# Optimization experiments

Hardware: AMD Instinct MI355X
Metric: run time of the kernel (lower is better)

## Reference

```python
import jax, jax.numpy as jnp
import numpy as np

B, S, D_MODEL = 2, 2048, 2048
HQ, HKV = 16, 8
HEAD_DIM = D_MODEL // HQ  # 128
ROPE_THETA = 10000.0


def setup_inputs() -> dict:
    key = jax.random.key(0)
    ks = jax.random.split(key, 5)
    scale = 1.0 / np.sqrt(D_MODEL)
    x = jax.random.normal(ks[0], (B, S, D_MODEL), dtype=jnp.float32)
    # torch nn.Linear weights: [out_features, in_features], no bias
    wq = jax.random.normal(ks[1], (HQ * HEAD_DIM, D_MODEL), dtype=jnp.float32) * scale
    wk = jax.random.normal(ks[2], (HKV * HEAD_DIM, D_MODEL), dtype=jnp.float32) * scale
    wv = jax.random.normal(ks[3], (HKV * HEAD_DIM, D_MODEL), dtype=jnp.float32) * scale
    wo = jax.random.normal(ks[4], (D_MODEL, HQ * HEAD_DIM), dtype=jnp.float32) * scale
    return {"x": x, "wq": wq, "wk": wk, "wv": wv, "wo": wo}


def _rope_tables(seq_len, head_dim, theta, dtype):
    # freqs = 1/theta^(2i/d); polar table equivalent to view_as_complex rotation
    inv = 1.0 / (theta ** (jnp.arange(0, head_dim, 2, dtype=jnp.float32) / head_dim))
    t = jnp.arange(seq_len, dtype=jnp.float32)
    ang = jnp.outer(t, inv)  # [S, head_dim//2]
    return jnp.cos(ang).astype(dtype), jnp.sin(ang).astype(dtype)


def _apply_rope(x, cos, sin):
    # x: [B, S, H, D]; complex pairs are interleaved (even=real, odd=imag)
    xr, xi = x[..., 0::2], x[..., 1::2]
    c = cos[None, :, None, :]
    s = sin[None, :, None, :]
    out_r = xr * c - xi * s
    out_i = xr * s + xi * c
    return jnp.stack([out_r, out_i], axis=-1).reshape(x.shape)


def reference(x, wq, wk, wv, wo):
    b, s, _ = x.shape
    q = (x @ wq.T).reshape(b, s, HQ, HEAD_DIM)
    k = (x @ wk.T).reshape(b, s, HKV, HEAD_DIM)
    v = (x @ wv.T).reshape(b, s, HKV, HEAD_DIM)

    cos, sin = _rope_tables(s, HEAD_DIM, ROPE_THETA, x.dtype)
    q = _apply_rope(q, cos, sin)
    k = _apply_rope(k, cos, sin)

    # [B, H, S, D]
    q = q.transpose(0, 2, 1, 3)
    k = k.transpose(0, 2, 1, 3)
    v = v.transpose(0, 2, 1, 3)
    # GQA: repeat kv heads to match query heads
    g = HQ // HKV
    k = jnp.repeat(k, g, axis=1)
    v = jnp.repeat(v, g, axis=1)

    scale = 1.0 / jnp.sqrt(jnp.asarray(HEAD_DIM, dtype=x.dtype))
    scores = jnp.einsum("bhqd,bhkd->bhqk", q, k) * scale
    causal = jnp.tril(jnp.ones((s, s), dtype=bool))
    scores = jnp.where(causal[None, None], scores, jnp.asarray(-jnp.inf, scores.dtype))
    attn = jax.nn.softmax(scores, axis=-1)
    out = jnp.einsum("bhqk,bhkd->bhqd", attn, v)  # [B, H, S, D]
    out = out.transpose(0, 2, 1, 3).reshape(b, s, HQ * HEAD_DIM)
    return out @ wo.T
```

## Files before the change

### kernel.cpp

```cpp
#include <hip/hip_runtime.h>

#define S_LEN 2048
#define DM    2048
#define HQ_N  16
#define HKV_N 8
#define HD    128

typedef unsigned short u16;
typedef unsigned int   u32;
typedef short bf16x8 __attribute__((ext_vector_type(8)));
typedef float f32x4  __attribute__((ext_vector_type(4)));
typedef u16   u16x8  __attribute__((ext_vector_type(8)));

__device__ __forceinline__ float b2f(u16 u) {
  u32 x = ((u32)u) << 16;
  return __builtin_bit_cast(float, x);
}
__device__ __forceinline__ u16 f2b(float f) {
  u32 u = __builtin_bit_cast(u32, f);
  u32 r = u + 0x7fffu + ((u >> 16) & 1u);
  return (u16)(r >> 16);
}

#define GLOAD_LDS16(g, l)                                                     \
  __builtin_amdgcn_global_load_lds(                                           \
      (const __attribute__((address_space(1))) void*)(g),                     \
      (__attribute__((address_space(3))) void*)(l), 16, 0, 0)

__global__ void cvt_bf16(const float* __restrict__ src, u16* __restrict__ dst) {
  int id = blockIdx.x * blockDim.x + threadIdx.x;
  float4 a = ((const float4*)src)[id * 2];
  float4 b = ((const float4*)src)[id * 2 + 1];
  u16x8 o;
  o[0] = f2b(a.x); o[1] = f2b(a.y); o[2] = f2b(a.z); o[3] = f2b(a.w);
  o[4] = f2b(b.x); o[5] = f2b(b.y); o[6] = f2b(b.z); o[7] = f2b(b.w);
  ((u16x8*)dst)[id] = o;
}

__global__ void rope_tables(float* __restrict__ cosT, float* __restrict__ sinT) {
  int id = blockIdx.x * blockDim.x + threadIdx.x;
  int t = id >> 6, i = id & 63;
  float inv = (float)pow(10000.0, -(double)(2 * i) / 128.0);
  float ang = (float)t * inv;
  cosT[id] = cosf(ang);
  sinT[id] = sinf(ang);
}

template <int EPI, int HH>
__global__ __launch_bounds__(256) void gemm_bt(const u16* __restrict__ A,
                                               const u16* __restrict__ W,
                                               void* __restrict__ Cv,
                                               int M, int N, int K) {
  __shared__ alignas(16) u16 As[128 * 32];
  __shared__ alignas(16) u16 Bs[128 * 32];
  const int tid  = threadIdx.x;
  const int lane = tid & 63;
  const int wave = tid >> 6;
  const int wr = (wave >> 1) * 64;
  const int wc = (wave & 1) * 64;
  const int bm = blockIdx.y * 128;
  const int bn = blockIdx.x * 128;
  const int r0 = tid >> 2;
  const int c0 = (tid & 3) * 8;
  u16* AsD = &As[tid * 8];
  u16* BsD = &Bs[tid * 8];
  const u16* Ap = A + (size_t)(bm + r0) * K + c0;
  const u16* Wp = W + (size_t)(bn + r0) * K + c0;
  const int cl = lane & 15;
  const int g8 = (lane >> 4) * 8;
  f32x4 acc[4][4] = {};
  for (int k0 = 0; k0 < K; k0 += 32) {
    __syncthreads();
    GLOAD_LDS16(Ap + k0, AsD);
    GLOAD_LDS16(Ap + (size_t)64 * K + k0, AsD + 2048);
    GLOAD_LDS16(Wp + k0, BsD);
    GLOAD_LDS16(Wp + (size_t)64 * K + k0, BsD + 2048);
    __syncthreads();
    bf16x8 af[4], bfr[4];
#pragma unroll
    for (int m = 0; m < 4; ++m)
      af[m] = *(const bf16x8*)&As[(wr + m * 16 + cl) * 32 + g8];
#pragma unroll
    for (int n = 0; n < 4; ++n)
      bfr[n] = *(const bf16x8*)&Bs[(wc + n * 16 + cl) * 32 + g8];
#pragma unroll
    for (int m = 0; m < 4; ++m)
#pragma unroll
      for (int n = 0; n < 4; ++n)
        acc[m][n] = __builtin_amdgcn_mfma_f32_16x16x32_bf16(af[m], bfr[n], acc[m][n], 0, 0, 0);
  }
  const int g4 = (lane >> 4) * 4;
#pragma unroll
  for (int m = 0; m < 4; ++m)
#pragma unroll
    for (int n = 0; n < 4; ++n)
#pragma unroll
      for (int r = 0; r < 4; ++r) {
        int row = bm + wr + m * 16 + g4 + r;
        int col = bn + wc + n * 16 + cl;
        float fv = acc[m][n][r];
        if (EPI == 3) {
          ((float*)Cv)[(size_t)row * N + col] = fv;
        } else if (EPI == 1) {
          int bb = row >> 11, s = row & (S_LEN - 1);
          int hk = col >> 7, d = col & (HD - 1);
          ((u16*)Cv)[((size_t)((bb * HKV_N + hk) * HD + d)) * S_LEN + s] = f2b(fv);
        } else {
          int bb = row >> 11, s = row & (S_LEN - 1);
          int h = col >> 7, d = col & (HD - 1);
          ((u16*)Cv)[((size_t)((bb * HH + h) * S_LEN + s)) * HD + d] = f2b(fv);
        }
      }
}

__global__ void rope_inplace(u16* __restrict__ buf,
                             const float* __restrict__ cosT,
                             const float* __restrict__ sinT, float scale) {
  int id = blockIdx.x * blockDim.x + threadIdx.x;
  int d0 = (id & 15) * 8;
  int rs = id >> 4;
  int s = rs & (S_LEN - 1);
  u16* p = buf + (size_t)rs * HD + d0;
  u16x8 v = *(const u16x8*)p;
  int p0 = d0 >> 1;
  float4 c  = *(const float4*)(cosT + s * 64 + p0);
  float4 sn = *(const float4*)(sinT + s * 64 + p0);
  float cc[4] = {c.x, c.y, c.z, c.w};
  float ss[4] = {sn.x, sn.y, sn.z, sn.w};
  u16x8 o;
#pragma unroll
  for (int j = 0; j < 4; ++j) {
    float x0 = b2f(v[2 * j]), x1 = b2f(v[2 * j + 1]);
    o[2 * j]     = f2b((x0 * cc[j] - x1 * ss[j]) * scale);
    o[2 * j + 1] = f2b((x0 * ss[j] + x1 * cc[j]) * scale);
  }
  *(u16x8*)p = o;
}

__global__ __launch_bounds__(256, 4) void attn_fwd(const u16* __restrict__ Q,
                                                   const u16* __restrict__ Kh,
                                                   const u16* __restrict__ Vt,
                                                   u16* __restrict__ O) {
  __shared__ alignas(16) u16 Ks[64 * 128];
  __shared__ alignas(16) u16 Vs[128 * 64];
  __shared__ alignas(16) u16 Plds[4][2][16 * 32];
  const int tid  = threadIdx.x;
  const int wave = tid >> 6;
  const int lane = tid & 63;
  const int orig = (blockIdx.x & 7) * 128 + (blockIdx.x >> 3);
  const int bh = orig >> 5;
  const int j = orig & 31;
  const int qblk = (j & 1) ? ((j - 1) >> 1) : (31 - (j >> 1));
  const int bb = bh >> 4, h = bh & 15;
  const int bkv = bb * HKV_N + (h >> 1);
  const u16* Kp = Kh + (size_t)bkv * S_LEN * HD;
  const u16* Vp = Vt + (size_t)bkv * HD * S_LEN;
  const int cl = lane & 15;
  const int gr = lane >> 4;
  const int g8 = gr * 8;
  const int sw8 = (cl & 7) << 3;
  const int q0w = qblk * 64 + wave * 16;
  const u16* Qp = Q + ((size_t)bh * S_LEN + q0w) * HD;
  bf16x8 qf[4];
#pragma unroll
  for (int c = 0; c < 4; ++c)
    qf[c] = *(const bf16x8*)&Qp[cl * HD + c * 32 + g8];
  const int krow_w = wave * 4 + gr;
  const int kcol = (cl * 8) ^ ((krow_w & 7) << 3);
  const u16* kSrc = Kp + (size_t)krow_w * HD + kcol;
  const int vrow_w = wave * 8 + (lane >> 3);
  const int vcol = ((lane & 7) * 8) ^ (((lane >> 3) & 7) << 3);
  const u16* vSrc = Vp + (size_t)vrow_w * S_LEN + vcol;
  float m[4]    = {-1e30f, -1e30f, -1e30f, -1e30f};
  float lsum[4] = {0.f, 0.f, 0.f, 0.f};
  f32x4 oacc[8] = {};
  u16* Pw0 = &Plds[wave][0][0];
  u16* Pw1 = &Plds[wave][1][0];
  for (int t = 0; t <= qblk; ++t) {
    const int k0 = t * 64;
    __syncthreads();
#pragma unroll
    for (int j2 = 0; j2 < 4; ++j2)
      GLOAD_LDS16(kSrc + (size_t)(k0 + j2 * 16) * HD, &Ks[(j2 * 4 + wave) * 512]);
#pragma unroll
    for (int j2 = 0; j2 < 4; ++j2)
      GLOAD_LDS16(vSrc + (size_t)j2 * 32 * S_LEN + k0, &Vs[(j2 * 4 + wave) * 512]);
    __syncthreads();
    f32x4 sc[4] = {{0.f, 0.f, 0.f, 0.f}, {0.f, 0.f, 0.f, 0.f},
                   {0.f, 0.f, 0.f, 0.f}, {0.f, 0.f, 0.f, 0.f}};
#pragma unroll
    for (int c = 0; c < 4; ++c) {
      const int kq = (c * 32 + g8) ^ sw8;
#pragma unroll
      for (int ks = 0; ks < 4; ++ks) {
        bf16x8 kf = *(const bf16x8*)&Ks[(ks * 16 + cl) * 128 + kq];
        sc[ks] = __builtin_amdgcn_mfma_f32_16x16x32_bf16(qf[c], kf, sc[ks], 0, 0, 0);
      }
    }
    float corr[4];
    if (t == qblk) {
#pragma unroll
      for (int r = 0; r < 4; ++r) {
        const int qrel = wave * 16 + gr * 4 + r;
#pragma unroll
        for (int ks = 0; ks < 4; ++ks)
          if (ks * 16 + cl > qrel) sc[ks][r] = -1e30f;
      }
    }
#pragma unroll
    for (int r = 0; r < 4; ++r) {
      float mx = fmaxf(fmaxf(sc[0][r], sc[1][r]), fmaxf(sc[2][r], sc[3][r]));
#pragma unroll
      for (int off = 1; off < 16; off <<= 1)
        mx = fmaxf(mx, __shfl_xor(mx, off));
      const float mn = fmaxf(m[r], mx);
      corr[r] = __expf(m[r] - mn);
      float p0 = __expf(sc[0][r] - mn);
      float p1 = __expf(sc[1][r] - mn);
      float p2 = __expf(sc[2][r] - mn);
      float p3 = __expf(sc[3][r] - mn);
      float rs = (p0 + p1) + (p2 + p3);
#pragma unroll
      for (int off = 1; off < 16; off <<= 1)
        rs += __shfl_xor(rs, off);
      lsum[r] = lsum[r] * corr[r] + rs;
      m[r] = mn;
      const int row = gr * 4 + r;
      Pw0[row * 32 + cl]      = f2b(p0);
      Pw0[row * 32 + 16 + cl] = f2b(p1);
      Pw1[row * 32 + cl]      = f2b(p2);
      Pw1[row * 32 + 16 + cl] = f2b(p3);
    }
#pragma unroll
    for (int nd = 0; nd < 8; ++nd)
#pragma unroll
      for (int r = 0; r < 4; ++r) oacc[nd][r] *= corr[r];
    __builtin_amdgcn_sched_barrier(0);
    asm volatile("s_waitcnt lgkmcnt(0)" ::: "memory");
    __builtin_amdgcn_sched_barrier(0);
    bf16x8 pa0 = *(const bf16x8*)&Pw0[cl * 32 + g8];
    bf16x8 pa1 = *(const bf16x8*)&Pw1[cl * 32 + g8];
    const int vq0 = g8 ^ sw8;
    const int vq1 = (32 + g8) ^ sw8;
#pragma unroll
    for (int nd = 0; nd < 8; ++nd) {
      bf16x8 vf0 = *(const bf16x8*)&Vs[(nd * 16 + cl) * 64 + vq0];
      bf16x8 vf1 = *(const bf16x8*)&Vs[(nd * 16 + cl) * 64 + vq1];
      oacc[nd] = __builtin_amdgcn_mfma_f32_16x16x32_bf16(pa0, vf0, oacc[nd], 0, 0, 0);
      oacc[nd] = __builtin_amdgcn_mfma_f32_16x16x32_bf16(pa1, vf1, oacc[nd], 0, 0, 0);
    }
  }
#pragma unroll
  for (int r = 0; r < 4; ++r) {
    const int q = q0w + gr * 4 + r;
    const float inv = 1.0f / lsum[r];
#pragma unroll
    for (int nd = 0; nd < 8; ++nd)
      O[(((size_t)bb * S_LEN + q) * HQ_N + h) * HD + nd * 16 + cl] =
          f2b(oacc[nd][r] * inv);
  }
}

extern "C" void kernel_launch(void* const* d_in, const int* in_sizes, int n_in,
                              void* d_out, int out_size, void* d_ws, size_t ws_size,
                              hipStream_t stream) {
  (void)in_sizes; (void)n_in; (void)out_size; (void)ws_size;
  const float* x  = (const float*)d_in[0];
  const float* wq = (const float*)d_in[1];
  const float* wk = (const float*)d_in[2];
  const float* wv = (const float*)d_in[3];
  const float* wo = (const float*)d_in[4];
  float* out = (float*)d_out;
  char* w = (char*)d_ws;
  u16*  Qh   = (u16*)(w + 0);
  u16*  Kh   = (u16*)(w + 16777216);
  u16*  Vt   = (u16*)(w + 25165824);
  u16*  x16  = (u16*)(w + 33554432);
  u16*  wq16 = (u16*)(w + 50331648);
  u16*  wk16 = (u16*)(w + 58720256);
  u16*  wv16 = (u16*)(w + 62914560);
  float* cosT = (float*)(w + 67108864);
  float* sinT = (float*)(w + 67633152);
  u16* wo16 = wq16;
  u16* attnout = x16;

  rope_tables<<<512, 256, 0, stream>>>(cosT, sinT);
  cvt_bf16<<<4096, 256, 0, stream>>>(x,  x16);
  cvt_bf16<<<2048, 256, 0, stream>>>(wq, wq16);
  cvt_bf16<<<1024, 256, 0, stream>>>(wk, wk16);
  cvt_bf16<<<1024, 256, 0, stream>>>(wv, wv16);
  gemm_bt<2, 16><<<dim3(16, 32), 256, 0, stream>>>(x16, wq16, Qh, 4096, 2048, 2048);
  gemm_bt<2, 8> <<<dim3(8, 32),  256, 0, stream>>>(x16, wk16, Kh, 4096, 1024, 2048);
  gemm_bt<1, 8> <<<dim3(8, 32),  256, 0, stream>>>(x16, wv16, Vt, 4096, 1024, 2048);
  cvt_bf16<<<2048, 256, 0, stream>>>(wo, wo16);
  rope_inplace<<<4096, 256, 0, stream>>>(Qh, cosT, sinT, 0.08838834764831845f);
  rope_inplace<<<2048, 256, 0, stream>>>(Kh, cosT, sinT, 1.0f);
  attn_fwd<<<1024, 256, 0, stream>>>(Qh, Kh, Vt, attnout);
  gemm_bt<3, 16><<<dim3(16, 32), 256, 0, stream>>>(attnout, wo16, out, 4096, 2048, 2048);
}
```

Baseline: 486.0 us.

## Fuse Q, K, V projections into one GEMM with XCD-aware block remap

Merges the three separate QKV projection GEMMs into a single launch over a concatenated bf16 weight buffer, with the epilogue routing each column block to the Q, K or V layout. Block indices are remapped so consecutive blocks spread across the 8 XCDs, which aims to improve L2 reuse of the shared A and W tiles. This removes two kernel launches and the tail effects of the smaller K/V grids. It adds branching in the epilogue and relies on the weights being contiguous in the workspace.

New measurement: 455.3 us. 6.3% less time.

```diff
diff --git a/kernel.cpp b/kernel.cpp
--- a/kernel.cpp
+++ b/kernel.cpp
@@ -46,11 +46,79 @@
   sinT[id] = sinf(ang);
 }
 
-template <int EPI, int HH>
-__global__ __launch_bounds__(256) void gemm_bt(const u16* __restrict__ A,
-                                               const u16* __restrict__ W,
-                                               void* __restrict__ Cv,
-                                               int M, int N, int K) {
+__global__ __launch_bounds__(256) void gemm_qkv(const u16* __restrict__ A,
+                                                const u16* __restrict__ W,
+                                                u16* __restrict__ Qh,
+                                                u16* __restrict__ Kh,
+                                                u16* __restrict__ Vt) {
+  __shared__ alignas(16) u16 As[128 * 32];
+  __shared__ alignas(16) u16 Bs[128 * 32];
+  const int K = DM;
+  const int tid  = threadIdx.x;
+  const int lane = tid & 63;
+  const int wave = tid >> 6;
+  const int wr = (wave >> 1) * 64;
+  const int wc = (wave & 1) * 64;
+  const int orig = (blockIdx.x & 7) * 128 + (blockIdx.x >> 3);
+  const int bn = (orig >> 5) * 128;
+  const int bm = (orig & 31) * 128;
+  const int r0 = tid >> 2;
+  const int c0 = (tid & 3) * 8;
+  u16* AsD = &As[tid * 8];
+  u16* BsD = &Bs[tid * 8];
+  const u16* Ap = A + (size_t)(bm + r0) * K + c0;
+  const u16* Wp = W + (size_t)(bn + r0) * K + c0;
+  const int cl = lane & 15;
+  const int g8 = (lane >> 4) * 8;
+  f32x4 acc[4][4] = {};
+  for (int k0 = 0; k0 < K; k0 += 32) {
+    __syncthreads();
+    GLOAD_LDS16(Ap + k0, AsD);
+    GLOAD_LDS16(Ap + (size_t)64 * K + k0, AsD + 2048);
+    GLOAD_LDS16(Wp + k0, BsD);
+    GLOAD_LDS16(Wp + (size_t)64 * K + k0, BsD + 2048);
+    __syncthreads();
+    bf16x8 af[4], bfr[4];
+#pragma unroll
+    for (int m = 0; m < 4; ++m)
+      af[m] = *(const bf16x8*)&As[(wr + m * 16 + cl) * 32 + g8];
+#pragma unroll
+    for (int n = 0; n < 4; ++n)
+      bfr[n] = *(const bf16x8*)&Bs[(wc + n * 16 + cl) * 32 + g8];
+#pragma unroll
+    for (int m = 0; m < 4; ++m)
+#pragma unroll
+      for (int n = 0; n < 4; ++n)
+        acc[m][n] = __builtin_amdgcn_mfma_f32_16x16x32_bf16(af[m], bfr[n], acc[m][n], 0, 0, 0);
+  }
+  const int g4 = (lane >> 4) * 4;
+#pragma unroll
+  for (int m = 0; m < 4; ++m)
+#pragma unroll
+    for (int n = 0; n < 4; ++n)
+#pragma unroll
+      for (int r = 0; r < 4; ++r) {
+        int row = bm + wr + m * 16 + g4 + r;
+        int col = bn + wc + n * 16 + cl;
+        int bb = row >> 11, s = row & (S_LEN - 1);
+        u16 v = f2b(acc[m][n][r]);
+        if (bn < 2048) {
+          int h = col >> 7, d = col & (HD - 1);
+          Qh[((size_t)((bb * HQ_N + h) * S_LEN + s)) * HD + d] = v;
+        } else if (bn < 3072) {
+          int hk = (col >> 7) - 16, d = col & (HD - 1);
+          Kh[((size_t)((bb * HKV_N + hk) * S_LEN + s)) * HD + d] = v;
+        } else {
+          int hk = (col >> 7) - 24, d = col & (HD - 1);
+          Vt[((size_t)((bb * HKV_N + hk) * HD + d)) * S_LEN + s] = v;
+        }
+      }
+}
+
+__global__ __launch_bounds__(256) void gemm_out(const u16* __restrict__ A,
+                                                const u16* __restrict__ W,
+                                                float* __restrict__ C,
+                                                int M, int N, int K) {
   __shared__ alignas(16) u16 As[128 * 32];
   __shared__ alignas(16) u16 Bs[128 * 32];
   const int tid  = threadIdx.x;
@@ -98,18 +166,7 @@
       for (int r = 0; r < 4; ++r) {
         int row = bm + wr + m * 16 + g4 + r;
         int col = bn + wc + n * 16 + cl;
-        float fv = acc[m][n][r];
-        if (EPI == 3) {
-          ((float*)Cv)[(size_t)row * N + col] = fv;
-        } else if (EPI == 1) {
-          int bb = row >> 11, s = row & (S_LEN - 1);
-          int hk = col >> 7, d = col & (HD - 1);
-          ((u16*)Cv)[((size_t)((bb * HKV_N + hk) * HD + d)) * S_LEN + s] = f2b(fv);
-        } else {
-          int bb = row >> 11, s = row & (S_LEN - 1);
-          int h = col >> 7, d = col & (HD - 1);
-          ((u16*)Cv)[((size_t)((bb * HH + h) * S_LEN + s)) * HD + d] = f2b(fv);
-        }
+        C[(size_t)row * N + col] = acc[m][n][r];
       }
 }
 
@@ -272,29 +329,25 @@
   const float* wo = (const float*)d_in[4];
   float* out = (float*)d_out;
   char* w = (char*)d_ws;
-  u16*  Qh   = (u16*)(w + 0);
-  u16*  Kh   = (u16*)(w + 16777216);
-  u16*  Vt   = (u16*)(w + 25165824);
-  u16*  x16  = (u16*)(w + 33554432);
-  u16*  wq16 = (u16*)(w + 50331648);
-  u16*  wk16 = (u16*)(w + 58720256);
-  u16*  wv16 = (u16*)(w + 62914560);
-  float* cosT = (float*)(w + 67108864);
-  float* sinT = (float*)(w + 67633152);
-  u16* wo16 = wq16;
+  u16*  Qh     = (u16*)(w + 0);
+  u16*  Kh     = (u16*)(w + 16777216);
+  u16*  Vt     = (u16*)(w + 25165824);
+  u16*  x16    = (u16*)(w + 33554432);
+  u16*  wqkv16 = (u16*)(w + 50331648);
+  float* cosT  = (float*)(w + 67108864);
+  float* sinT  = (float*)(w + 67633152);
+  u16* wo16 = wqkv16;
   u16* attnout = x16;
 
   rope_tables<<<512, 256, 0, stream>>>(cosT, sinT);
   cvt_bf16<<<4096, 256, 0, stream>>>(x,  x16);
-  cvt_bf16<<<2048, 256, 0, stream>>>(wq, wq16);
-  cvt_bf16<<<1024, 256, 0, stream>>>(wk, wk16);
-  cvt_bf16<<<1024, 256, 0, stream>>>(wv, wv16);
-  gemm_bt<2, 16><<<dim3(16, 32), 256, 0, stream>>>(x16, wq16, Qh, 4096, 2048, 2048);
-  gemm_bt<2, 8> <<<dim3(8, 32),  256, 0, stream>>>(x16, wk16, Kh, 4096, 1024, 2048);
-  gemm_bt<1, 8> <<<dim3(8, 32),  256, 0, stream>>>(x16, wv16, Vt, 4096, 1024, 2048);
+  cvt_bf16<<<2048, 256, 0, stream>>>(wq, wqkv16);
+  cvt_bf16<<<1024, 256, 0, stream>>>(wk, wqkv16 + 2048 * 2048);
+  cvt_bf16<<<1024, 256, 0, stream>>>(wv, wqkv16 + 3072 * 2048);
+  gemm_qkv<<<1024, 256, 0, stream>>>(x16, wqkv16, Qh, Kh, Vt);
   cvt_bf16<<<2048, 256, 0, stream>>>(wo, wo16);
   rope_inplace<<<4096, 256, 0, stream>>>(Qh, cosT, sinT, 0.08838834764831845f);
   rope_inplace<<<2048, 256, 0, stream>>>(Kh, cosT, sinT, 1.0f);
   attn_fwd<<<1024, 256, 0, stream>>>(Qh, Kh, Vt, attnout);
-  gemm_bt<3, 16><<<dim3(16, 32), 256, 0, stream>>>(attnout, wo16, out, 4096, 2048, 2048);
-}
+  gemm_out<<<dim3(16, 32), 256, 0, stream>>>(attnout, wo16, out, 4096, 2048, 2048);
+}
```
